# Performance work log

Hardware: AMD Instinct MI355X
Metric: run time of the kernel (lower is better)

Reference implementation:

```python
import jax, jax.numpy as jnp
import numpy as np

SOS = 1

def _gru_cell(x, h, Wih, Whh, bih, bhh):
    # PyTorch GRU cell: gates ordered (r, z, n)
    gi = x @ Wih.T + bih
    gh = h @ Whh.T + bhh
    ir, iz, inn = jnp.split(gi, 3, axis=-1)
    hr, hz, hn = jnp.split(gh, 3, axis=-1)
    r = jax.nn.sigmoid(ir + hr)
    z = jax.nn.sigmoid(iz + hz)
    n = jnp.tanh(inn + r * hn)
    return (1.0 - z) * n + z * h


def setup_inputs() -> dict:
    key = jax.random.key(0)
    ks = jax.random.split(key, 17)
    V, E, H, Lin, Tout, B, Lmax = 50000, 512, 512, 400, 100, 64, 400
    s = 0.05
    f = jax.random.normal
    return {
        "emb":     f(ks[0], (V, E)) * s,
        "enc_Wih": f(ks[1], (3 * H, E)) * s,
        "enc_Whh": f(ks[2], (3 * H, H)) * s,
        "enc_bih": f(ks[3], (3 * H,)) * s,
        "enc_bhh": f(ks[4], (3 * H,)) * s,
        "attn_W":  f(ks[5], (Lmax, 2 * H)) * s,
        "attn_b":  f(ks[6], (Lmax,)) * s,
        "comb_W":  f(ks[7], (H, 2 * H)) * s,
        "comb_b":  f(ks[8], (H,)) * s,
        "dec_Wih": f(ks[9], (3 * H, H)) * s,
        "dec_Whh": f(ks[10], (3 * H, H)) * s,
        "dec_bih": f(ks[11], (3 * H,)) * s,
        "dec_bhh": f(ks[12], (3 * H,)) * s,
        "out_W":   f(ks[13], (V, H)) * s,
        "out_b":   f(ks[14], (V,)) * s,
        "input_tensor":  jax.random.randint(ks[15], (Lin, B), 0, V),
        "target_tensor": jax.random.randint(ks[16], (Tout, B), 0, V),
    }


def reference(emb, enc_Wih, enc_Whh, enc_bih, enc_bhh, attn_W, attn_b,
              comb_W, comb_b, dec_Wih, dec_Whh, dec_bih, dec_bhh,
              out_W, out_b, input_tensor, target_tensor):
    B = input_tensor.shape[1]
    H = enc_Whh.shape[1]

    # ---- encoder: 1-layer GRU over [L, B, E] ----
    enc_x = emb[input_tensor]                      # [L, B, E]
    h0 = jnp.zeros((B, H), enc_x.dtype)
    def enc_step(h, x):
        h2 = _gru_cell(x, h, enc_Wih, enc_Whh, enc_bih, enc_bhh)
        return h2, h2
    h_enc, enc_out = jax.lax.scan(enc_step, h0, enc_x)   # enc_out: [L, B, H]
    enc0 = enc_out[0]                              # [B, H]; source's attn_applied[0] picks timestep 0

    # ---- decoder: teacher-forced, NLLLoss(mean) summed over steps ----
    dec_tokens = jnp.concatenate(
        [jnp.full((1, B), SOS, target_tensor.dtype), target_tensor[:-1]], axis=0)
    dec_x = emb[dec_tokens]                        # [T, B, H] (embed_size == hidden_size)

    def dec_step(h, xt):
        x, tgt = xt                                # x: [B, H], tgt: [B]
        a = jax.nn.softmax(jnp.concatenate([x, h], 1) @ attn_W.T + attn_b, axis=1)  # [B, Lmax]
        # faithful to source: elementwise broadcast picks enc_out[0] scaled by a[:, 0]
        ctx = enc0 * a[:, :1]                      # [B, H]
        c = jax.nn.relu(jnp.concatenate([x, ctx], 1) @ comb_W.T + comb_b)           # [B, H]
        h2 = _gru_cell(c, h, dec_Wih, dec_Whh, dec_bih, dec_bhh)
        logp = jax.nn.log_softmax(h2 @ out_W.T + out_b, axis=1)                     # [B, V]
        loss_t = -jnp.mean(jnp.take_along_axis(logp, tgt[:, None], axis=1))
        return h2, loss_t

    _, losses = jax.lax.scan(dec_step, h_enc, (dec_x, target_tensor))
    return jnp.sum(losses)
```

## Files before the change

### kernel.cpp

```cpp
#include <hip/hip_runtime.h>
#include <math.h>


typedef __attribute__((ext_vector_type(8))) short bh8;
typedef __attribute__((ext_vector_type(4))) float fv4;

__device__ __forceinline__ float b2f(short u) {
    union { unsigned int i; float f; } c;
    c.i = ((unsigned int)(unsigned short)u) << 16;
    return c.f;
}
__device__ __forceinline__ short f2b(float f) {
    union { float f; unsigned int u; } c;
    c.f = f;
    unsigned int r = (c.u + 0x7fffu + ((c.u >> 16) & 1u)) >> 16;
    return (short)r;
}
__device__ __forceinline__ bh8 ld8(const float* __restrict__ p) {
    bh8 r;
    #pragma unroll
    for (int j = 0; j < 8; ++j) r[j] = f2b(p[j]);
    return r;
}
__device__ __forceinline__ float sigmf(float x) { return 1.f / (1.f + expf(-x)); }

__device__ __forceinline__ fv4 mfma16(bh8 a, bh8 b, fv4 c) {
    return __builtin_amdgcn_mfma_f32_16x16x32_bf16(a, b, c, 0, 0, 0);
}

__device__ __forceinline__ void gridbar(unsigned int* bar, unsigned int target) {
    __syncthreads();
    if (threadIdx.x == 0) {
        __hip_atomic_fetch_add(bar, 1u, __ATOMIC_RELEASE, __HIP_MEMORY_SCOPE_AGENT);
        while (__hip_atomic_fetch_add(bar, 0u, __ATOMIC_RELAXED,
                                      __HIP_MEMORY_SCOPE_AGENT) < target) {
            __builtin_amdgcn_s_sleep(16);
        }
        __builtin_amdgcn_fence(__ATOMIC_ACQUIRE, "agent");
    }
    __syncthreads();
}

__global__ __launch_bounds__(256) void k_cvt(
    const float* __restrict__ s, short* __restrict__ d, int n)
{
    const int i = (blockIdx.x * 256 + threadIdx.x) * 4;
    if (i + 3 < n) {
        fv4 v = *(const fv4*)(s + i);
        short4 o;
        o.x = f2b(v[0]); o.y = f2b(v[1]); o.z = f2b(v[2]); o.w = f2b(v[3]);
        *(short4*)(d + i) = o;
    }
}

__global__ __launch_bounds__(256) void k_enc_persist(
    const float* __restrict__ emb, const int* __restrict__ input_t,
    const short* __restrict__ Wb,
    const float* __restrict__ Wih_f, const float* __restrict__ Whh_f,
    const float* __restrict__ bih, const float* __restrict__ bhh,
    float* __restrict__ h_f32, short* __restrict__ h_bf,
    float* __restrict__ enc0, unsigned int* __restrict__ bar)
{
    const int tid  = threadIdx.x;
    const int lane = tid & 63;
    const int wv   = tid >> 6;
    const int n0   = blockIdx.x * 16;
    const int b0   = wv * 16;
    const int l15  = lane & 15;
    const int ko   = lane >> 4;
    const int koff = ko * 8;
    const int brow = b0 + l15;
    const int n    = n0 + l15;

    for (int i = blockIdx.x * 256 + tid; i < 64 * 512; i += 32 * 256) {
        h_f32[i] = 0.f; h_bf[i] = 0;
    }
    gridbar(bar, 32u);

    const bh8 *Wrb = nullptr, *Wzb = nullptr, *Wnb = nullptr;
    const bh8 *Urb = nullptr, *Uzb = nullptr, *Unb = nullptr;
    const float *Wrf = nullptr, *Wzf = nullptr, *Wnf = nullptr;
    const float *Urf = nullptr, *Uzf = nullptr, *Unf = nullptr;
    if (Wb) {
        Wrb = (const bh8*)(Wb + (long long)(n + 0)    * 512) + ko;
        Wzb = (const bh8*)(Wb + (long long)(n + 512)  * 512) + ko;
        Wnb = (const bh8*)(Wb + (long long)(n + 1024) * 512) + ko;
        Urb = (const bh8*)(Wb + (long long)(n + 1536) * 512) + ko;
        Uzb = (const bh8*)(Wb + (long long)(n + 2048) * 512) + ko;
        Unb = (const bh8*)(Wb + (long long)(n + 2560) * 512) + ko;
    } else {
        Wrf = Wih_f + (long long)(n + 0)    * 512 + koff;
        Wzf = Wih_f + (long long)(n + 512)  * 512 + koff;
        Wnf = Wih_f + (long long)(n + 1024) * 512 + koff;
        Urf = Whh_f + (long long)(n + 0)    * 512 + koff;
        Uzf = Whh_f + (long long)(n + 512)  * 512 + koff;
        Unf = Whh_f + (long long)(n + 1024) * 512 + koff;
    }
    const float bir = bih[n], biz = bih[n + 512], bin = bih[n + 1024];
    const float bhr = bhh[n], bhz = bhh[n + 512], bhn = bhh[n + 1024];

    for (int t = 0; t < 400; ++t) {
        const float* hi  = h_f32 + (t & 1) * 32768;
        const short* hib = h_bf  + (t & 1) * 32768;
        float* ho  = h_f32 + ((t + 1) & 1) * 32768;
        short* hob = h_bf  + ((t + 1) & 1) * 32768;

        const int tok = input_t[t * 64 + brow];
        const float* Ap = emb + (long long)tok * 512 + koff;
        const bh8*  Hp  = (const bh8*)(hib + (long long)brow * 512) + ko;

        fv4 air = {0.f, 0.f, 0.f, 0.f};
        fv4 aiz = air, ain = air, ahr = air, ahz = air, ahn = air;
        if (Wb) {
            #pragma unroll 4
            for (int kk = 0; kk < 16; ++kk) {
                const bh8 a = ld8(Ap + kk * 32);
                const bh8 h = Hp[kk * 4];
                air = mfma16(a, Wrb[kk * 4], air);
                aiz = mfma16(a, Wzb[kk * 4], aiz);
                ain = mfma16(a, Wnb[kk * 4], ain);
                ahr = mfma16(h, Urb[kk * 4], ahr);
                ahz = mfma16(h, Uzb[kk * 4], ahz);
                ahn = mfma16(h, Unb[kk * 4], ahn);
            }
        } else {
            #pragma unroll 4
            for (int kk = 0; kk < 16; ++kk) {
                const bh8 a = ld8(Ap + kk * 32);
                const bh8 h = Hp[kk * 4];
                air = mfma16(a, ld8(Wrf + kk * 32), air);
                aiz = mfma16(a, ld8(Wzf + kk * 32), aiz);
                ain = mfma16(a, ld8(Wnf + kk * 32), ain);
                ahr = mfma16(h, ld8(Urf + kk * 32), ahr);
                ahz = mfma16(h, ld8(Uzf + kk * 32), ahz);
                ahn = mfma16(h, ld8(Unf + kk * 32), ahn);
            }
        }
        #pragma unroll
        for (int r = 0; r < 4; ++r) {
            const int b = b0 + ko * 4 + r;
            const float rr = sigmf(air[r] + bir + ahr[r] + bhr);
            const float zz = sigmf(aiz[r] + biz + ahz[r] + bhz);
            const float nn = tanhf(ain[r] + bin + rr * (ahn[r] + bhn));
            const float hold = hi[b * 512 + n];
            const float hnew = (1.f - zz) * nn + zz * hold;
            ho[b * 512 + n] = hnew;
            hob[b * 512 + n] = f2b(hnew);
            if (t == 0) enc0[b * 512 + n] = hnew;
        }
        gridbar(bar, 32u * (t + 2));
    }
}

struct SmAB { float sx[1024]; float red[256]; float red2[256]; };
struct SmD  { float sl[64][65]; };
union SMem { SmAB ab; SmD d; };

__device__ __forceinline__ void dec_lossred(
    const float* __restrict__ pm, const float* __restrict__ ps,
    const float* __restrict__ tlog, float* __restrict__ lacc,
    float* red, float* red2, int r, int tid)
{
    float m = -1e30f, s = 0.f;
    for (int i = tid; i < 782; i += 256) {
        const float m2 = pm[i * 64 + r];
        const float s2 = ps[i * 64 + r];
        if (m2 > m) { s = s * expf(m - m2) + s2; m = m2; }
        else        { s += s2 * expf(m2 - m); }
    }
    red[tid] = m; red2[tid] = s;
    __syncthreads();
    for (int st = 128; st > 0; st >>= 1) {
        if (tid < st) {
            const float m2 = red[tid + st], s2 = red2[tid + st];
            const float M = fmaxf(red[tid], m2);
            red2[tid] = red2[tid] * expf(red[tid] - M) + s2 * expf(m2 - M);
            red[tid] = M;
        }
        __syncthreads();
    }
    if (tid == 0) {
        const float logp = tlog[r] - (red[0] + logf(red2[0]));
        atomicAdd(lacc, -logp * (1.f / 64.f));
    }
    __syncthreads();
}

__global__ __launch_bounds__(256) void k_dec_persist(
    const float* __restrict__ emb, const float* __restrict__ enc0,
    const float* __restrict__ attn_W, const float* __restrict__ attn_b,
    const float* __restrict__ comb_W, const float* __restrict__ comb_b,
    const short* __restrict__ decWb,
    const float* __restrict__ dec_Wih, const float* __restrict__ dec_Whh,
    const float* __restrict__ dec_bih, const float* __restrict__ dec_bhh,
    const short* __restrict__ outWb, const float* __restrict__ outW,
    const float* __restrict__ outb, const int* __restrict__ target,
    float* __restrict__ h_f32, short* __restrict__ h_bf,
    short* __restrict__ c_bf, float* __restrict__ scores,
    float* __restrict__ pm, float* __restrict__ ps,
    float* __restrict__ tlog, float* __restrict__ lacc,
    unsigned int* __restrict__ bar2)
{
    __shared__ SMem sm;
    const int tid = threadIdx.x;
    const int bid = blockIdx.x;
    const int r   = bid >> 2;
    const int q   = bid & 3;
    unsigned int tgt = 0u;

    for (int t = 0; t < 100; ++t) {
        const float* hi  = h_f32 + (t & 1) * 32768;
        const short* hib = h_bf  + (t & 1) * 32768;
        float* ho  = h_f32 + ((t + 1) & 1) * 32768;
        short* hob = h_bf  + ((t + 1) & 1) * 32768;

        const int tok = (t == 0) ? 1 : target[(t - 1) * 64 + r];
        for (int k = tid; k < 512; k += 256) {
            sm.ab.sx[k]       = emb[(long long)tok * 512 + k];
            sm.ab.sx[512 + k] = hi[r * 512 + k];
        }
        if (q == 0 && t > 0)
            dec_lossred(pm, ps, tlog, lacc, sm.ab.red, sm.ab.red2, r, tid);
        __syncthreads();
        if (tid < 100) {
            const int nn = q * 100 + tid;
            const fv4* wrow = (const fv4*)(attn_W + (long long)nn * 1024);
            float s0 = 0.f, s1 = 0.f, s2 = 0.f, s3 = 0.f;
            for (int kc = 0; kc < 256; ++kc) {
                fv4 v = wrow[kc];
                s0 += v[0] * sm.ab.sx[kc * 4 + 0];
                s1 += v[1] * sm.ab.sx[kc * 4 + 1];
                s2 += v[2] * sm.ab.sx[kc * 4 + 2];
                s3 += v[3] * sm.ab.sx[kc * 4 + 3];
            }
            scores[r * 400 + nn] = (s0 + s1) + (s2 + s3) + attn_b[nn];
        }
        tgt += 256u; gridbar(bar2, tgt);

        {
            float m = -1e30f;
            for (int i = tid; i < 400; i += 256) m = fmaxf(m, scores[r * 400 + i]);
            sm.ab.red[tid] = m;
            __syncthreads();
            for (int st = 128; st > 0; st >>= 1) {
                if (tid < st) sm.ab.red[tid] = fmaxf(sm.ab.red[tid], sm.ab.red[tid + st]);
                __syncthreads();
            }
            m = sm.ab.red[0];
            __syncthreads();
            float ssum = 0.f;
            for (int i = tid; i < 400; i += 256) ssum += expf(scores[r * 400 + i] - m);
            sm.ab.red2[tid] = ssum;
            __syncthreads();
            for (int st = 128; st > 0; st >>= 1) {
                if (tid < st) sm.ab.red2[tid] += sm.ab.red2[tid + st];
                __syncthreads();
            }
            const float a0 = expf(scores[r * 400 + 0] - m) / sm.ab.red2[0];
            __syncthreads();
            for (int k = tid; k < 512; k += 256)
                sm.ab.sx[512 + k] = enc0[r * 512 + k] * a0;
            __syncthreads();
        }
        if (tid < 128) {
            const int j = q * 128 + tid;
            const fv4* wrow = (const fv4*)(comb_W + (long long)j * 1024);
            float s0 = 0.f, s1 = 0.f, s2 = 0.f, s3 = 0.f;
            for (int kc = 0; kc < 256; ++kc) {
                fv4 v = wrow[kc];
                s0 += v[0] * sm.ab.sx[kc * 4 + 0];
                s1 += v[1] * sm.ab.sx[kc * 4 + 1];
                s2 += v[2] * sm.ab.sx[kc * 4 + 2];
                s3 += v[3] * sm.ab.sx[kc * 4 + 3];
            }
            const float acc = (s0 + s1) + (s2 + s3) + comb_b[j];
            c_bf[r * 512 + j] = f2b(fmaxf(acc, 0.f));
        }
        tgt += 256u; gridbar(bar2, tgt);

        if (bid < 32) {
            const int lane = tid & 63;
            const int w    = bid * 4 + (tid >> 6);
            const int b0g  = (w & 3) * 16;
            const int n0g  = (w >> 2) * 16;
            const int l15  = lane & 15;
            const int ko   = lane >> 4;
            const int koff = ko * 8;
            const int brow = b0g + l15;
            const int n    = n0g + l15;

            const bh8* Ap = (const bh8*)(c_bf + (long long)brow * 512) + ko;
            const bh8* Hp = (const bh8*)(hib + (long long)brow * 512) + ko;

            fv4 air = {0.f, 0.f, 0.f, 0.f};
            fv4 aiz = air, ain = air, ahr = air, ahz = air, ahn = air;
            if (decWb) {
                const bh8* Wr = (const bh8*)(decWb + (long long)(n + 0)    * 512) + ko;
                const bh8* Wz = (const bh8*)(decWb + (long long)(n + 512)  * 512) + ko;
                const bh8* Wn = (const bh8*)(decWb + (long long)(n + 1024) * 512) + ko;
                const bh8* Ur = (const bh8*)(decWb + (long long)(n + 1536) * 512) + ko;
                const bh8* Uz = (const bh8*)(decWb + (long long)(n + 2048) * 512) + ko;
                const bh8* Un = (const bh8*)(decWb + (long long)(n + 2560) * 512) + ko;
                #pragma unroll 4
                for (int kk = 0; kk < 16; ++kk) {
                    const bh8 a = Ap[kk * 4];
                    const bh8 h = Hp[kk * 4];
                    air = mfma16(a, Wr[kk * 4], air);
                    aiz = mfma16(a, Wz[kk * 4], aiz);
                    ain = mfma16(a, Wn[kk * 4], ain);
                    ahr = mfma16(h, Ur[kk * 4], ahr);
                    ahz = mfma16(h, Uz[kk * 4], ahz);
                    ahn = mfma16(h, Un[kk * 4], ahn);
                }
            } else {
                const float* Wr = dec_Wih + (long long)(n + 0)    * 512 + koff;
                const float* Wz = dec_Wih + (long long)(n + 512)  * 512 + koff;
                const float* Wn = dec_Wih + (long long)(n + 1024) * 512 + koff;
                const float* Ur = dec_Whh + (long long)(n + 0)    * 512 + koff;
                const float* Uz = dec_Whh + (long long)(n + 512)  * 512 + koff;
                const float* Un = dec_Whh + (long long)(n + 1024) * 512 + koff;
                #pragma unroll 4
                for (int kk = 0; kk < 16; ++kk) {
                    const bh8 a = Ap[kk * 4];
                    const bh8 h = Hp[kk * 4];
                    air = mfma16(a, ld8(Wr + kk * 32), air);
                    aiz = mfma16(a, ld8(Wz + kk * 32), aiz);
                    ain = mfma16(a, ld8(Wn + kk * 32), ain);
                    ahr = mfma16(h, ld8(Ur + kk * 32), ahr);
                    ahz = mfma16(h, ld8(Uz + kk * 32), ahz);
                    ahn = mfma16(h, ld8(Un + kk * 32), ahn);
                }
            }
            const float bir = dec_bih[n], biz = dec_bih[n + 512], bin = dec_bih[n + 1024];
            const float bhr = dec_bhh[n], bhz = dec_bhh[n + 512], bhn = dec_bhh[n + 1024];
            #pragma unroll
            for (int rr = 0; rr < 4; ++rr) {
                const int b = b0g + ko * 4 + rr;
                const float rg = sigmf(air[rr] + bir + ahr[rr] + bhr);
                const float zg = sigmf(aiz[rr] + biz + ahz[rr] + bhz);
                const float ng = tanhf(ain[rr] + bin + rg * (ahn[rr] + bhn));
                const float hold = hi[b * 512 + n];
                const float hnew = (1.f - zg) * ng + zg * hold;
                ho[b * 512 + n] = hnew;
                hob[b * 512 + n] = f2b(hnew);
            }
        }
        tgt += 256u; gridbar(bar2, tgt);

        for (int ch = bid; ch < 782; ch += 256) {
            const int lane = tid & 63;
            const int wl   = tid >> 6;
            const int base = ch * 64;
            const int n0c  = base + wl * 16;
            const int l15  = lane & 15;
            const int ko   = lane >> 4;
            const int v    = n0c + l15;
            const int vcl  = (v < 50000) ? v : 49999;
            const bh8* A0 = (const bh8*)(hob + (long long)(0  + l15) * 512) + ko;
            const bh8* A1 = (const bh8*)(hob + (long long)(16 + l15) * 512) + ko;
            const bh8* A2 = (const bh8*)(hob + (long long)(32 + l15) * 512) + ko;
            const bh8* A3 = (const bh8*)(hob + (long long)(48 + l15) * 512) + ko;

            bh8 bb[16];
            if (outWb) {
                const bh8* Bp = (const bh8*)(outWb + (long long)vcl * 512) + ko;
                #pragma unroll
                for (int kk = 0; kk < 16; ++kk) bb[kk] = Bp[kk * 4];
            } else {
                const float* Bp = outW + (long long)vcl * 512 + ko * 8;
                #pragma unroll
                for (int kk = 0; kk < 16; ++kk) bb[kk] = ld8(Bp + kk * 32);
            }
            fv4 c0 = {0.f, 0.f, 0.f, 0.f};
            fv4 c1 = c0, c2 = c0, c3 = c0;
            #pragma unroll
            for (int kk = 0; kk < 16; ++kk) {
                c0 = mfma16(A0[kk * 4], bb[kk], c0);
                c1 = mfma16(A1[kk * 4], bb[kk], c1);
                c2 = mfma16(A2[kk * 4], bb[kk], c2);
                c3 = mfma16(A3[kk * 4], bb[kk], c3);
            }
            const float bv = outb[vcl];
            const int cc = wl * 16 + l15;
            const bool ok = (v < 50000);
            #pragma unroll
            for (int rr = 0; rr < 4; ++rr) {
                const int row = ko * 4 + rr;
                sm.d.sl[0  + row][cc] = ok ? (c0[rr] + bv) : -1e30f;
                sm.d.sl[16 + row][cc] = ok ? (c1[rr] + bv) : -1e30f;
                sm.d.sl[32 + row][cc] = ok ? (c2[rr] + bv) : -1e30f;
                sm.d.sl[48 + row][cc] = ok ? (c3[rr] + bv) : -1e30f;
            }
            __syncthreads();
            if (tid < 64) {
                const int b = tid;
                float m = -1e30f, s = 0.f;
                for (int cj = 0; cj < 64; ++cj) {
                    const float x = sm.d.sl[b][cj];
                    if (x > m) { s = s * expf(m - x) + 1.f; m = x; }
                    else       { s += expf(x - m); }
                }
                pm[ch * 64 + b] = m;
                ps[ch * 64 + b] = s;
                const int tg = target[t * 64 + b];
                const int rel = tg - base;
                if (rel >= 0 && rel < 64) tlog[b] = sm.d.sl[b][rel];
            }
            __syncthreads();
        }
        tgt += 256u; gridbar(bar2, tgt);
    }

    if (q == 0)
        dec_lossred(pm, ps, tlog, lacc, sm.ab.red, sm.ab.red2, r, tid);
}

__global__ __launch_bounds__(256) void k_gru1(
    const short* __restrict__ c_bf, const short* __restrict__ Wb,
    const float* __restrict__ Wih_f, const float* __restrict__ Whh_f,
    const float* __restrict__ bih, const float* __restrict__ bhh,
    const float* __restrict__ hi, const short* __restrict__ hib,
    float* __restrict__ ho, short* __restrict__ hob)
{
    const int tid  = threadIdx.x;
    const int lane = tid & 63;
    const int w    = blockIdx.x * 4 + (tid >> 6);
    const int b0   = (w & 3) * 16;
    const int n0   = (w >> 2) * 16;
    const int l15  = lane & 15;
    const int ko   = lane >> 4;
    const int koff = ko * 8;
    const int brow = b0 + l15;
    const int n    = n0 + l15;

    const bh8* Ap = (const bh8*)(c_bf + (long long)brow * 512) + ko;
    const bh8* Hp = (const bh8*)(hib + (long long)brow * 512) + ko;

    fv4 air = {0.f, 0.f, 0.f, 0.f};
    fv4 aiz = air, ain = air, ahr = air, ahz = air, ahn = air;
    if (Wb) {
        const bh8* Wr = (const bh8*)(Wb + (long long)(n + 0)    * 512) + ko;
        const bh8* Wz = (const bh8*)(Wb + (long long)(n + 512)  * 512) + ko;
        const bh8* Wn = (const bh8*)(Wb + (long long)(n + 1024) * 512) + ko;
        const bh8* Ur = (const bh8*)(Wb + (long long)(n + 1536) * 512) + ko;
        const bh8* Uz = (const bh8*)(Wb + (long long)(n + 2048) * 512) + ko;
        const bh8* Un = (const bh8*)(Wb + (long long)(n + 2560) * 512) + ko;
        #pragma unroll 4
        for (int kk = 0; kk < 16; ++kk) {
            const bh8 a = Ap[kk * 4];
            const bh8 h = Hp[kk * 4];
            air = mfma16(a, Wr[kk * 4], air);
            aiz = mfma16(a, Wz[kk * 4], aiz);
            ain = mfma16(a, Wn[kk * 4], ain);
            ahr = mfma16(h, Ur[kk * 4], ahr);
            ahz = mfma16(h, Uz[kk * 4], ahz);
            ahn = mfma16(h, Un[kk * 4], ahn);
        }
    } else {
        const float* Wr = Wih_f + (long long)(n + 0)    * 512 + koff;
        const float* Wz = Wih_f + (long long)(n + 512)  * 512 + koff;
        const float* Wn = Wih_f + (long long)(n + 1024) * 512 + koff;
        const float* Ur = Whh_f + (long long)(n + 0)    * 512 + koff;
        const float* Uz = Whh_f + (long long)(n + 512)  * 512 + koff;
        const float* Un = Whh_f + (long long)(n + 1024) * 512 + koff;
        #pragma unroll 4
        for (int kk = 0; kk < 16; ++kk) {
            const bh8 a = Ap[kk * 4];
            const bh8 h = Hp[kk * 4];
            air = mfma16(a, ld8(Wr + kk * 32), air);
            aiz = mfma16(a, ld8(Wz + kk * 32), aiz);
            ain = mfma16(a, ld8(Wn + kk * 32), ain);
            ahr = mfma16(h, ld8(Ur + kk * 32), ahr);
            ahz = mfma16(h, ld8(Uz + kk * 32), ahz);
            ahn = mfma16(h, ld8(Un + kk * 32), ahn);
        }
    }
    const float bir = bih[n], biz = bih[n + 512], bin = bih[n + 1024];
    const float bhr = bhh[n], bhz = bhh[n + 512], bhn = bhh[n + 1024];
    #pragma unroll
    for (int r = 0; r < 4; ++r) {
        const int b = b0 + ko * 4 + r;
        const float rr = sigmf(air[r] + bir + ahr[r] + bhr);
        const float zz = sigmf(aiz[r] + biz + ahz[r] + bhz);
        const float nn = tanhf(ain[r] + bin + rr * (ahn[r] + bhn));
        const float hold = hi[b * 512 + n];
        const float hnew = (1.f - zz) * nn + zz * hold;
        ho[b * 512 + n] = hnew;
        hob[b * 512 + n] = f2b(hnew);
    }
}

__global__ __launch_bounds__(256) void k_attncomb(
    const float* __restrict__ emb, const float* __restrict__ h_f32,
    const float* __restrict__ enc0,
    const float* __restrict__ attn_W, const float* __restrict__ attn_b,
    const float* __restrict__ comb_W, const float* __restrict__ comb_b,
    const int* __restrict__ target, int td, short* __restrict__ c_bf)
{
    __shared__ float sx[1024];
    __shared__ float sc[400];
    __shared__ float red[256];
    __shared__ float a0s;
    const int b = blockIdx.x;
    const int tid = threadIdx.x;
    const int tok = (td == 0) ? 1 : target[(td - 1) * 64 + b];
    for (int k = tid; k < 512; k += 256) {
        sx[k] = emb[(long long)tok * 512 + k];
        sx[512 + k] = h_f32[b * 512 + k];
    }
    __syncthreads();
    for (int nn = tid; nn < 400; nn += 256) {
        const fv4* wrow = (const fv4*)(attn_W + (long long)nn * 1024);
        float acc = 0.f;
        for (int kc = 0; kc < 256; ++kc) {
            fv4 v = wrow[kc];
            acc += v[0] * sx[kc * 4 + 0] + v[1] * sx[kc * 4 + 1]
                 + v[2] * sx[kc * 4 + 2] + v[3] * sx[kc * 4 + 3];
        }
        sc[nn] = acc + attn_b[nn];
    }
    __syncthreads();
    float m = -1e30f;
    for (int nn = tid; nn < 400; nn += 256) m = fmaxf(m, sc[nn]);
    red[tid] = m;
    __syncthreads();
    for (int s = 128; s > 0; s >>= 1) {
        if (tid < s) red[tid] = fmaxf(red[tid], red[tid + s]);
        __syncthreads();
    }
    m = red[0];
    __syncthreads();
    float ss = 0.f;
    for (int nn = tid; nn < 400; nn += 256) ss += expf(sc[nn] - m);
    red[tid] = ss;
    __syncthreads();
    for (int s = 128; s > 0; s >>= 1) {
        if (tid < s) red[tid] += red[tid + s];
        __syncthreads();
    }
    if (tid == 0) a0s = expf(sc[0] - m) / red[0];
    __syncthreads();
    const float a0b = a0s;
    for (int k = tid; k < 512; k += 256) sx[512 + k] = enc0[b * 512 + k] * a0b;
    __syncthreads();
    for (int j = tid; j < 512; j += 256) {
        const fv4* wrow = (const fv4*)(comb_W + (long long)j * 1024);
        float acc = 0.f;
        for (int kc = 0; kc < 256; ++kc) {
            fv4 v = wrow[kc];
            acc += v[0] * sx[kc * 4 + 0] + v[1] * sx[kc * 4 + 1]
                 + v[2] * sx[kc * 4 + 2] + v[3] * sx[kc * 4 + 3];
        }
        acc += comb_b[j];
        c_bf[b * 512 + j] = f2b(fmaxf(acc, 0.f));
    }
}

__global__ __launch_bounds__(256) void k_outloss(
    const short* __restrict__ h2bf,
    const short* __restrict__ outWb, const float* __restrict__ outW,
    const float* __restrict__ outb, const int* __restrict__ target,
    float* __restrict__ pm, float* __restrict__ ps, float* __restrict__ tlogit)
{
    __shared__ float sl[64][65];
    const int tid  = threadIdx.x;
    const int lane = tid & 63;
    const int wl   = tid >> 6;
    const int base = blockIdx.x * 64;
    const int n0   = base + wl * 16;
    const int l15  = lane & 15;
    const int ko   = lane >> 4;

    const int v    = n0 + l15;
    const int vcl  = (v < 50000) ? v : 49999;
    const bh8* A0 = (const bh8*)(h2bf + (long long)(0  + l15) * 512) + ko;
    const bh8* A1 = (const bh8*)(h2bf + (long long)(16 + l15) * 512) + ko;
    const bh8* A2 = (const bh8*)(h2bf + (long long)(32 + l15) * 512) + ko;
    const bh8* A3 = (const bh8*)(h2bf + (long long)(48 + l15) * 512) + ko;
    fv4 c0 = {0.f, 0.f, 0.f, 0.f};
    fv4 c1 = c0, c2 = c0, c3 = c0;
    if (outWb) {
        const bh8* Bp = (const bh8*)(outWb + (long long)vcl * 512) + ko;
        #pragma unroll 4
        for (int kk = 0; kk < 16; ++kk) {
            const bh8 bb = Bp[kk * 4];
            c0 = mfma16(A0[kk * 4], bb, c0);
            c1 = mfma16(A1[kk * 4], bb, c1);
            c2 = mfma16(A2[kk * 4], bb, c2);
            c3 = mfma16(A3[kk * 4], bb, c3);
        }
    } else {
        const float* Bp = outW + (long long)vcl * 512 + ko * 8;
        #pragma unroll 4
        for (int kk = 0; kk < 16; ++kk) {
            const bh8 bb = ld8(Bp + kk * 32);
            c0 = mfma16(A0[kk * 4], bb, c0);
            c1 = mfma16(A1[kk * 4], bb, c1);
            c2 = mfma16(A2[kk * 4], bb, c2);
            c3 = mfma16(A3[kk * 4], bb, c3);
        }
    }
    const float bv = outb[vcl];
    const int cc = wl * 16 + l15;
    const bool ok = (v < 50000);
    #pragma unroll
    for (int r = 0; r < 4; ++r) {
        const int row = ko * 4 + r;
        sl[0  + row][cc] = ok ? (c0[r] + bv) : -1e30f;
        sl[16 + row][cc] = ok ? (c1[r] + bv) : -1e30f;
        sl[32 + row][cc] = ok ? (c2[r] + bv) : -1e30f;
        sl[48 + row][cc] = ok ? (c3[r] + bv) : -1e30f;
    }
    __syncthreads();
    if (tid < 64) {
        const int b = tid;
        float m = -1e30f, s = 0.f;
        for (int c = 0; c < 64; ++c) {
            const float x = sl[b][c];
            if (x > m) { s = s * expf(m - x) + 1.f; m = x; }
            else       { s += expf(x - m); }
        }
        pm[blockIdx.x * 64 + b] = m;
        ps[blockIdx.x * 64 + b] = s;
        const int tg = target[b];
        const int rel = tg - base;
        if (rel >= 0 && rel < 64) tlogit[b] = sl[b][rel];
    }
}

__global__ __launch_bounds__(256) void k_lossred(
    const float* __restrict__ pm, const float* __restrict__ ps,
    const float* __restrict__ tlogit, float* __restrict__ loss_acc)
{
    __shared__ float rm[256], rs[256];
    const int b = blockIdx.x;
    const int tid = threadIdx.x;
    float m = -1e30f, s = 0.f;
    for (int i = tid; i < 782; i += 256) {
        const float m2 = pm[i * 64 + b];
        const float s2 = ps[i * 64 + b];
        if (m2 > m) { s = s * expf(m - m2) + s2; m = m2; }
        else        { s += s2 * expf(m2 - m); }
    }
    rm[tid] = m; rs[tid] = s;
    __syncthreads();
    for (int st = 128; st > 0; st >>= 1) {
        if (tid < st) {
            const float m2 = rm[tid + st], s2 = rs[tid + st];
            const float M = fmaxf(rm[tid], m2);
            rs[tid] = rs[tid] * expf(rm[tid] - M) + s2 * expf(m2 - M);
            rm[tid] = M;
        }
        __syncthreads();
    }
    if (tid == 0) {
        const float logp = tlogit[b] - (rm[0] + logf(rs[0]));
        atomicAdd(loss_acc, -logp * (1.f / 64.f));
    }
}

__global__ void k_init(float* h_f32_0, short* h_bf_0, float* loss_acc,
                       unsigned int* bar, unsigned int* bar2)
{
    const int i = blockIdx.x * 256 + threadIdx.x;
    if (i < 64 * 512) { h_f32_0[i] = 0.f; h_bf_0[i] = 0; }
    if (i == 0) { *loss_acc = 0.f; *bar = 0u; *bar2 = 0u; }
}

__global__ void k_final(const float* loss_acc, float* out)
{
    out[0] = *loss_acc;
}

extern "C" void kernel_launch(void* const* d_in, const int* in_sizes, int n_in,
                              void* d_out, int out_size, void* d_ws, size_t ws_size,
                              hipStream_t stream)
{
    const float* emb     = (const float*)d_in[0];
    const float* enc_Wih = (const float*)d_in[1];
    const float* enc_Whh = (const float*)d_in[2];
    const float* enc_bih = (const float*)d_in[3];
    const float* enc_bhh = (const float*)d_in[4];
    const float* attn_W  = (const float*)d_in[5];
    const float* attn_b  = (const float*)d_in[6];
    const float* comb_W  = (const float*)d_in[7];
    const float* comb_b  = (const float*)d_in[8];
    const float* dec_Wih = (const float*)d_in[9];
    const float* dec_Whh = (const float*)d_in[10];
    const float* dec_bih = (const float*)d_in[11];
    const float* dec_bhh = (const float*)d_in[12];
    const float* out_W   = (const float*)d_in[13];
    const float* out_b   = (const float*)d_in[14];
    const int*   input_t = (const int*)d_in[15];
    const int*   target_t= (const int*)d_in[16];

    char* ws = (char*)d_ws;
    float* h_f32  = (float*)(ws + 0);
    float* enc0   = (float*)(ws + 262144);
    short* h_bf   = (short*)(ws + 393216);
    short* c_bf   = (short*)(ws + 524288);
    float* lacc   = (float*)(ws + 589824);
    unsigned int* bar  = (unsigned int*)(ws + 590080);
    unsigned int* bar2 = (unsigned int*)(ws + 590208);
    float* pm     = (float*)(ws + 590336);
    float* ps     = (float*)(ws + 790528);
    float* tlog   = (float*)(ws + 990720);
    short* encWb  = (short*)(ws + 990976);
    float* scores = (float*)(ws + 990976);
    short* decWb  = (short*)(ws + 4136704);
    short* outWb  = (short*)(ws + 7282432);

    const bool tier1 = ws_size >= 7282432;
    const bool tier2 = ws_size >= 58482432;
    const bool fuse  = ws_size >= 1093376;

    k_init<<<128, 256, 0, stream>>>(h_f32, h_bf, lacc, bar, bar2);

    if (tier1) {
        k_cvt<<<768, 256, 0, stream>>>(enc_Wih, encWb, 786432);
        k_cvt<<<768, 256, 0, stream>>>(enc_Whh, encWb + 786432, 786432);
        k_cvt<<<768, 256, 0, stream>>>(dec_Wih, decWb, 786432);
        k_cvt<<<768, 256, 0, stream>>>(dec_Whh, decWb + 786432, 786432);
    }
    if (tier2) {
        k_cvt<<<25000, 256, 0, stream>>>(out_W, outWb, 25600000);
    }

    k_enc_persist<<<32, 256, 0, stream>>>(
        emb, input_t, tier1 ? encWb : nullptr, enc_Wih, enc_Whh,
        enc_bih, enc_bhh, h_f32, h_bf, enc0, bar);

    if (fuse) {
        k_dec_persist<<<256, 256, 0, stream>>>(
            emb, enc0, attn_W, attn_b, comb_W, comb_b,
            tier1 ? decWb : nullptr, dec_Wih, dec_Whh, dec_bih, dec_bhh,
            tier2 ? outWb : nullptr, out_W, out_b, target_t,
            h_f32, h_bf, c_bf, scores, pm, ps, tlog, lacc, bar2);
    } else {
        for (int td = 0; td < 100; ++td) {
            const float* hi  = h_f32 + (td & 1) * 32768;
            const short* hib = h_bf  + (td & 1) * 32768;
            float* ho  = h_f32 + ((td + 1) & 1) * 32768;
            short* hob = h_bf  + ((td + 1) & 1) * 32768;
            k_attncomb<<<64, 256, 0, stream>>>(emb, hi, enc0, attn_W, attn_b,
                                               comb_W, comb_b, target_t, td, c_bf);
            k_gru1<<<32, 256, 0, stream>>>(c_bf, tier1 ? decWb : nullptr,
                                           dec_Wih, dec_Whh, dec_bih, dec_bhh,
                                           hi, hib, ho, hob);
            k_outloss<<<782, 256, 0, stream>>>(hob, tier2 ? outWb : nullptr, out_W,
                                               out_b, target_t + td * 64,
                                               pm, ps, tlog);
            k_lossred<<<64, 256, 0, stream>>>(pm, ps, tlog, lacc);
        }
    }

    k_final<<<1, 1, 0, stream>>>(lacc, (float*)d_out);
}
```

Measured before the change: 28.27 ms.

## Move output projection out of recurrent loop into one batched kernel over all steps

The persistent decoder now runs only the recurrent part (attention, combine, GRU) on 64 blocks with two grid barriers per step, and stores every step's hidden state in bf16. A separate kernel then computes the vocabulary projection and partial log-softmax for all 100 steps in parallel (800 blocks). A final kernel reduces the partial results into the loss. This removes the huge per-step vocabulary GEMM and its barriers from the serial critical path. It also converts only part of out_W to bf16 under a smaller workspace budget and falls back to fp32 loads for the remaining chunks.

```diff
diff --git a/kernel.cpp b/kernel.cpp
--- a/kernel.cpp
+++ b/kernel.cpp
@@ -4,6 +4,9 @@
 
 typedef __attribute__((ext_vector_type(8))) short bh8;
 typedef __attribute__((ext_vector_type(4))) float fv4;
+
+#define NSL 8
+#define CONVCH 640
 
 __device__ __forceinline__ float b2f(short u) {
     union { unsigned int i; float f; } c;
@@ -152,131 +155,88 @@
     }
 }
 
-struct SmAB { float sx[1024]; float red[256]; float red2[256]; };
-struct SmD  { float sl[64][65]; };
-union SMem { SmAB ab; SmD d; };
-
-__device__ __forceinline__ void dec_lossred(
-    const float* __restrict__ pm, const float* __restrict__ ps,
-    const float* __restrict__ tlog, float* __restrict__ lacc,
-    float* red, float* red2, int r, int tid)
-{
-    float m = -1e30f, s = 0.f;
-    for (int i = tid; i < 782; i += 256) {
-        const float m2 = pm[i * 64 + r];
-        const float s2 = ps[i * 64 + r];
-        if (m2 > m) { s = s * expf(m - m2) + s2; m = m2; }
-        else        { s += s2 * expf(m2 - m); }
-    }
-    red[tid] = m; red2[tid] = s;
-    __syncthreads();
-    for (int st = 128; st > 0; st >>= 1) {
-        if (tid < st) {
-            const float m2 = red[tid + st], s2 = red2[tid + st];
-            const float M = fmaxf(red[tid], m2);
-            red2[tid] = red2[tid] * expf(red[tid] - M) + s2 * expf(m2 - M);
-            red[tid] = M;
-        }
-        __syncthreads();
-    }
-    if (tid == 0) {
-        const float logp = tlog[r] - (red[0] + logf(red2[0]));
-        atomicAdd(lacc, -logp * (1.f / 64.f));
-    }
-    __syncthreads();
-}
-
-__global__ __launch_bounds__(256) void k_dec_persist(
+__global__ __launch_bounds__(256) void k_dec2(
     const float* __restrict__ emb, const float* __restrict__ enc0,
     const float* __restrict__ attn_W, const float* __restrict__ attn_b,
     const float* __restrict__ comb_W, const float* __restrict__ comb_b,
     const short* __restrict__ decWb,
     const float* __restrict__ dec_Wih, const float* __restrict__ dec_Whh,
     const float* __restrict__ dec_bih, const float* __restrict__ dec_bhh,
-    const short* __restrict__ outWb, const float* __restrict__ outW,
-    const float* __restrict__ outb, const int* __restrict__ target,
-    float* __restrict__ h_f32, short* __restrict__ h_bf,
-    short* __restrict__ c_bf, float* __restrict__ scores,
-    float* __restrict__ pm, float* __restrict__ ps,
-    float* __restrict__ tlog, float* __restrict__ lacc,
+    const int* __restrict__ target,
+    float* __restrict__ h,
+    const float* __restrict__ h0,
+    const short* __restrict__ h0b,
+    short* __restrict__ c_bf, short* __restrict__ Hall,
     unsigned int* __restrict__ bar2)
 {
-    __shared__ SMem sm;
+    __shared__ __align__(16) float sx[1024];
+    __shared__ float sc[400];
+    __shared__ float red[256];
+    __shared__ float a0s;
     const int tid = threadIdx.x;
     const int bid = blockIdx.x;
-    const int r   = bid >> 2;
-    const int q   = bid & 3;
     unsigned int tgt = 0u;
 
     for (int t = 0; t < 100; ++t) {
-        const float* hi  = h_f32 + (t & 1) * 32768;
-        const short* hib = h_bf  + (t & 1) * 32768;
-        float* ho  = h_f32 + ((t + 1) & 1) * 32768;
-        short* hob = h_bf  + ((t + 1) & 1) * 32768;
-
-        const int tok = (t == 0) ? 1 : target[(t - 1) * 64 + r];
-        for (int k = tid; k < 512; k += 256) {
-            sm.ab.sx[k]       = emb[(long long)tok * 512 + k];
-            sm.ab.sx[512 + k] = hi[r * 512 + k];
-        }
-        if (q == 0 && t > 0)
-            dec_lossred(pm, ps, tlog, lacc, sm.ab.red, sm.ab.red2, r, tid);
-        __syncthreads();
-        if (tid < 100) {
-            const int nn = q * 100 + tid;
-            const fv4* wrow = (const fv4*)(attn_W + (long long)nn * 1024);
-            float s0 = 0.f, s1 = 0.f, s2 = 0.f, s3 = 0.f;
-            for (int kc = 0; kc < 256; ++kc) {
-                fv4 v = wrow[kc];
-                s0 += v[0] * sm.ab.sx[kc * 4 + 0];
-                s1 += v[1] * sm.ab.sx[kc * 4 + 1];
-                s2 += v[2] * sm.ab.sx[kc * 4 + 2];
-                s3 += v[3] * sm.ab.sx[kc * 4 + 3];
-            }
-            scores[r * 400 + nn] = (s0 + s1) + (s2 + s3) + attn_b[nn];
-        }
-        tgt += 256u; gridbar(bar2, tgt);
-
         {
+            const int r = bid;
+            const float* hsrc = (t == 0) ? h0 : h;
+            const int tok = (t == 0) ? 1 : target[(t - 1) * 64 + r];
+            for (int k = tid; k < 512; k += 256) {
+                sx[k]       = emb[(long long)tok * 512 + k];
+                sx[512 + k] = hsrc[r * 512 + k];
+            }
+            __syncthreads();
+            for (int nn = tid; nn < 400; nn += 256) {
+                const fv4* wrow = (const fv4*)(attn_W + (long long)nn * 1024);
+                float s0 = 0.f, s1 = 0.f, s2 = 0.f, s3 = 0.f;
+                for (int kc = 0; kc < 256; ++kc) {
+                    const fv4 v = wrow[kc];
+                    const fv4 xv = *(const fv4*)(sx + kc * 4);
+                    s0 += v[0] * xv[0]; s1 += v[1] * xv[1];
+                    s2 += v[2] * xv[2]; s3 += v[3] * xv[3];
+                }
+                sc[nn] = (s0 + s1) + (s2 + s3) + attn_b[nn];
+            }
+            __syncthreads();
             float m = -1e30f;
-            for (int i = tid; i < 400; i += 256) m = fmaxf(m, scores[r * 400 + i]);
-            sm.ab.red[tid] = m;
+            for (int nn = tid; nn < 400; nn += 256) m = fmaxf(m, sc[nn]);
+            red[tid] = m;
             __syncthreads();
-            for (int st = 128; st > 0; st >>= 1) {
-                if (tid < st) sm.ab.red[tid] = fmaxf(sm.ab.red[tid], sm.ab.red[tid + st]);
+            for (int s = 128; s > 0; s >>= 1) {
+                if (tid < s) red[tid] = fmaxf(red[tid], red[tid + s]);
                 __syncthreads();
             }
-            m = sm.ab.red[0];
+            m = red[0];
             __syncthreads();
-            float ssum = 0.f;
-            for (int i = tid; i < 400; i += 256) ssum += expf(scores[r * 400 + i] - m);
-            sm.ab.red2[tid] = ssum;
+            float ss = 0.f;
+            for (int nn = tid; nn < 400; nn += 256) ss += expf(sc[nn] - m);
+            red[tid] = ss;
             __syncthreads();
-            for (int st = 128; st > 0; st >>= 1) {
-                if (tid < st) sm.ab.red2[tid] += sm.ab.red2[tid + st];
+            for (int s = 128; s > 0; s >>= 1) {
+                if (tid < s) red[tid] += red[tid + s];
                 __syncthreads();
             }
-            const float a0 = expf(scores[r * 400 + 0] - m) / sm.ab.red2[0];
+            if (tid == 0) a0s = expf(sc[0] - m) / red[0];
             __syncthreads();
+            const float a0 = a0s;
             for (int k = tid; k < 512; k += 256)
-                sm.ab.sx[512 + k] = enc0[r * 512 + k] * a0;
+                sx[512 + k] = enc0[r * 512 + k] * a0;
             __syncthreads();
-        }
-        if (tid < 128) {
-            const int j = q * 128 + tid;
-            const fv4* wrow = (const fv4*)(comb_W + (long long)j * 1024);
-            float s0 = 0.f, s1 = 0.f, s2 = 0.f, s3 = 0.f;
-            for (int kc = 0; kc < 256; ++kc) {
-                fv4 v = wrow[kc];
-                s0 += v[0] * sm.ab.sx[kc * 4 + 0];
-                s1 += v[1] * sm.ab.sx[kc * 4 + 1];
-                s2 += v[2] * sm.ab.sx[kc * 4 + 2];
-                s3 += v[3] * sm.ab.sx[kc * 4 + 3];
-            }
-            const float acc = (s0 + s1) + (s2 + s3) + comb_b[j];
-            c_bf[r * 512 + j] = f2b(fmaxf(acc, 0.f));
-        }
-        tgt += 256u; gridbar(bar2, tgt);
+            for (int j = tid; j < 512; j += 256) {
+                const fv4* wrow = (const fv4*)(comb_W + (long long)j * 1024);
+                float s0 = 0.f, s1 = 0.f, s2 = 0.f, s3 = 0.f;
+                for (int kc = 0; kc < 256; ++kc) {
+                    const fv4 v = wrow[kc];
+                    const fv4 xv = *(const fv4*)(sx + kc * 4);
+                    s0 += v[0] * xv[0]; s1 += v[1] * xv[1];
+                    s2 += v[2] * xv[2]; s3 += v[3] * xv[3];
+                }
+                const float acc = (s0 + s1) + (s2 + s3) + comb_b[j];
+                c_bf[r * 512 + j] = f2b(fmaxf(acc, 0.f));
+            }
+        }
+        tgt += 64u; gridbar(bar2, tgt);
 
         if (bid < 32) {
             const int lane = tid & 63;
@@ -289,8 +249,10 @@
             const int brow = b0g + l15;
             const int n    = n0g + l15;
 
+            const short* Hprev = (t == 0) ? h0b : (Hall + (long long)(t - 1) * 32768);
+            const float* hsrc  = (t == 0) ? h0  : h;
             const bh8* Ap = (const bh8*)(c_bf + (long long)brow * 512) + ko;
-            const bh8* Hp = (const bh8*)(hib + (long long)brow * 512) + ko;
+            const bh8* Hp = (const bh8*)(Hprev + (long long)brow * 512) + ko;
 
             fv4 air = {0.f, 0.f, 0.f, 0.f};
             fv4 aiz = air, ain = air, ahr = air, ahz = air, ahn = air;
@@ -304,13 +266,13 @@
                 #pragma unroll 4
                 for (int kk = 0; kk < 16; ++kk) {
                     const bh8 a = Ap[kk * 4];
-                    const bh8 h = Hp[kk * 4];
-                    air = mfma16(a, Wr[kk * 4], air);
-                    aiz = mfma16(a, Wz[kk * 4], aiz);
-                    ain = mfma16(a, Wn[kk * 4], ain);
-                    ahr = mfma16(h, Ur[kk * 4], ahr);
-                    ahz = mfma16(h, Uz[kk * 4], ahz);
-                    ahn = mfma16(h, Un[kk * 4], ahn);
+                    const bh8 hh = Hp[kk * 4];
+                    air = mfma16(a,  Wr[kk * 4], air);
+                    aiz = mfma16(a,  Wz[kk * 4], aiz);
+                    ain = mfma16(a,  Wn[kk * 4], ain);
+                    ahr = mfma16(hh, Ur[kk * 4], ahr);
+                    ahz = mfma16(hh, Uz[kk * 4], ahz);
+                    ahn = mfma16(hh, Un[kk * 4], ahn);
                 }
             } else {
                 const float* Wr = dec_Wih + (long long)(n + 0)    * 512 + koff;
@@ -322,97 +284,149 @@
                 #pragma unroll 4
                 for (int kk = 0; kk < 16; ++kk) {
                     const bh8 a = Ap[kk * 4];
-                    const bh8 h = Hp[kk * 4];
-                    air = mfma16(a, ld8(Wr + kk * 32), air);
-                    aiz = mfma16(a, ld8(Wz + kk * 32), aiz);
-                    ain = mfma16(a, ld8(Wn + kk * 32), ain);
-                    ahr = mfma16(h, ld8(Ur + kk * 32), ahr);
-                    ahz = mfma16(h, ld8(Uz + kk * 32), ahz);
-                    ahn = mfma16(h, ld8(Un + kk * 32), ahn);
+                    const bh8 hh = Hp[kk * 4];
+                    air = mfma16(a,  ld8(Wr + kk * 32), air);
+                    aiz = mfma16(a,  ld8(Wz + kk * 32), aiz);
+                    ain = mfma16(a,  ld8(Wn + kk * 32), ain);
+                    ahr = mfma16(hh, ld8(Ur + kk * 32), ahr);
+                    ahz = mfma16(hh, ld8(Uz + kk * 32), ahz);
+                    ahn = mfma16(hh, ld8(Un + kk * 32), ahn);
                 }
             }
             const float bir = dec_bih[n], biz = dec_bih[n + 512], bin = dec_bih[n + 1024];
             const float bhr = dec_bhh[n], bhz = dec_bhh[n + 512], bhn = dec_bhh[n + 1024];
+            short* Ht = Hall + (long long)t * 32768;
             #pragma unroll
             for (int rr = 0; rr < 4; ++rr) {
                 const int b = b0g + ko * 4 + rr;
                 const float rg = sigmf(air[rr] + bir + ahr[rr] + bhr);
                 const float zg = sigmf(aiz[rr] + biz + ahz[rr] + bhz);
                 const float ng = tanhf(ain[rr] + bin + rg * (ahn[rr] + bhn));
-                const float hold = hi[b * 512 + n];
+                const float hold = hsrc[b * 512 + n];
                 const float hnew = (1.f - zg) * ng + zg * hold;
-                ho[b * 512 + n] = hnew;
-                hob[b * 512 + n] = f2b(hnew);
-            }
-        }
-        tgt += 256u; gridbar(bar2, tgt);
-
-        for (int ch = bid; ch < 782; ch += 256) {
-            const int lane = tid & 63;
-            const int wl   = tid >> 6;
-            const int base = ch * 64;
-            const int n0c  = base + wl * 16;
-            const int l15  = lane & 15;
-            const int ko   = lane >> 4;
-            const int v    = n0c + l15;
-            const int vcl  = (v < 50000) ? v : 49999;
-            const bh8* A0 = (const bh8*)(hob + (long long)(0  + l15) * 512) + ko;
-            const bh8* A1 = (const bh8*)(hob + (long long)(16 + l15) * 512) + ko;
-            const bh8* A2 = (const bh8*)(hob + (long long)(32 + l15) * 512) + ko;
-            const bh8* A3 = (const bh8*)(hob + (long long)(48 + l15) * 512) + ko;
-
-            bh8 bb[16];
-            if (outWb) {
-                const bh8* Bp = (const bh8*)(outWb + (long long)vcl * 512) + ko;
-                #pragma unroll
-                for (int kk = 0; kk < 16; ++kk) bb[kk] = Bp[kk * 4];
-            } else {
-                const float* Bp = outW + (long long)vcl * 512 + ko * 8;
-                #pragma unroll
-                for (int kk = 0; kk < 16; ++kk) bb[kk] = ld8(Bp + kk * 32);
-            }
-            fv4 c0 = {0.f, 0.f, 0.f, 0.f};
-            fv4 c1 = c0, c2 = c0, c3 = c0;
+                h[b * 512 + n] = hnew;
+                Ht[b * 512 + n] = f2b(hnew);
+            }
+        }
+        tgt += 64u; gridbar(bar2, tgt);
+    }
+}
+
+__global__ __launch_bounds__(256) void k_outbatch(
+    const short* __restrict__ Hall,
+    const short* __restrict__ outWb, const float* __restrict__ outW,
+    const float* __restrict__ outb, const int* __restrict__ target,
+    float* __restrict__ pm2, float* __restrict__ ps2, float* __restrict__ tlog2)
+{
+    __shared__ float sl[64][65];
+    __shared__ float mm[4][64], sm[4][64], tm[4][64];
+    const int tid  = threadIdx.x;
+    const int s    = blockIdx.x & 7;
+    const int t    = blockIdx.x >> 3;
+    const int lane = tid & 63;
+    const int wl   = tid >> 6;
+    const int l15  = lane & 15;
+    const int ko   = lane >> 4;
+    const short* Ht = Hall + (long long)t * 32768;
+    const bh8* A0 = (const bh8*)(Ht + (long long)(0  + l15) * 512) + ko;
+    const bh8* A1 = (const bh8*)(Ht + (long long)(16 + l15) * 512) + ko;
+    const bh8* A2 = (const bh8*)(Ht + (long long)(32 + l15) * 512) + ko;
+    const bh8* A3 = (const bh8*)(Ht + (long long)(48 + l15) * 512) + ko;
+
+    const int row = tid & 63;
+    const int seg = tid >> 6;
+    const int tg  = target[t * 64 + row];
+    float lm = -1e30f, ls = 0.f, tcap = -1e30f;
+
+    const int ch0 = s * 98;
+    const int ch1 = (ch0 + 98 < 782) ? (ch0 + 98) : 782;
+    for (int ch = ch0; ch < ch1; ++ch) {
+        const int base = ch * 64;
+        const int n0c  = base + wl * 16;
+        const int v    = n0c + l15;
+        const int vcl  = (v < 50000) ? v : 49999;
+        bh8 bb[16];
+        if (outWb && ch < CONVCH) {
+            const bh8* Bp = (const bh8*)(outWb + (long long)vcl * 512) + ko;
             #pragma unroll
-            for (int kk = 0; kk < 16; ++kk) {
-                c0 = mfma16(A0[kk * 4], bb[kk], c0);
-                c1 = mfma16(A1[kk * 4], bb[kk], c1);
-                c2 = mfma16(A2[kk * 4], bb[kk], c2);
-                c3 = mfma16(A3[kk * 4], bb[kk], c3);
-            }
-            const float bv = outb[vcl];
-            const int cc = wl * 16 + l15;
-            const bool ok = (v < 50000);
+            for (int kk = 0; kk < 16; ++kk) bb[kk] = Bp[kk * 4];
+        } else {
+            const float* Bp = outW + (long long)vcl * 512 + ko * 8;
             #pragma unroll
-            for (int rr = 0; rr < 4; ++rr) {
-                const int row = ko * 4 + rr;
-                sm.d.sl[0  + row][cc] = ok ? (c0[rr] + bv) : -1e30f;
-                sm.d.sl[16 + row][cc] = ok ? (c1[rr] + bv) : -1e30f;
-                sm.d.sl[32 + row][cc] = ok ? (c2[rr] + bv) : -1e30f;
-                sm.d.sl[48 + row][cc] = ok ? (c3[rr] + bv) : -1e30f;
-            }
-            __syncthreads();
-            if (tid < 64) {
-                const int b = tid;
-                float m = -1e30f, s = 0.f;
-                for (int cj = 0; cj < 64; ++cj) {
-                    const float x = sm.d.sl[b][cj];
-                    if (x > m) { s = s * expf(m - x) + 1.f; m = x; }
-                    else       { s += expf(x - m); }
-                }
-                pm[ch * 64 + b] = m;
-                ps[ch * 64 + b] = s;
-                const int tg = target[t * 64 + b];
-                const int rel = tg - base;
-                if (rel >= 0 && rel < 64) tlog[b] = sm.d.sl[b][rel];
-            }
-            __syncthreads();
-        }
-        tgt += 256u; gridbar(bar2, tgt);
-    }
-
-    if (q == 0)
-        dec_lossred(pm, ps, tlog, lacc, sm.ab.red, sm.ab.red2, r, tid);
+            for (int kk = 0; kk < 16; ++kk) bb[kk] = ld8(Bp + kk * 32);
+        }
+        fv4 c0 = {0.f, 0.f, 0.f, 0.f};
+        fv4 c1 = c0, c2 = c0, c3 = c0;
+        #pragma unroll
+        for (int kk = 0; kk < 16; ++kk) {
+            c0 = mfma16(A0[kk * 4], bb[kk], c0);
+            c1 = mfma16(A1[kk * 4], bb[kk], c1);
+            c2 = mfma16(A2[kk * 4], bb[kk], c2);
+            c3 = mfma16(A3[kk * 4], bb[kk], c3);
+        }
+        const float bv = outb[vcl];
+        const int cc = wl * 16 + l15;
+        const bool ok = (v < 50000);
+        #pragma unroll
+        for (int rr = 0; rr < 4; ++rr) {
+            const int rw = ko * 4 + rr;
+            sl[0  + rw][cc] = ok ? (c0[rr] + bv) : -1e30f;
+            sl[16 + rw][cc] = ok ? (c1[rr] + bv) : -1e30f;
+            sl[32 + rw][cc] = ok ? (c2[rr] + bv) : -1e30f;
+            sl[48 + rw][cc] = ok ? (c3[rr] + bv) : -1e30f;
+        }
+        __syncthreads();
+        #pragma unroll
+        for (int j = 0; j < 16; ++j) {
+            const float x = sl[row][seg * 16 + j];
+            if (x > lm) { ls = ls * expf(lm - x) + 1.f; lm = x; }
+            else        { ls += expf(x - lm); }
+            if (base + seg * 16 + j == tg) tcap = x;
+        }
+        __syncthreads();
+    }
+    mm[seg][row] = lm; sm[seg][row] = ls; tm[seg][row] = tcap;
+    __syncthreads();
+    if (tid < 64) {
+        float M = mm[0][tid], S = sm[0][tid], T = tm[0][tid];
+        #pragma unroll
+        for (int g = 1; g < 4; ++g) {
+            const float m2 = mm[g][tid], s2 = sm[g][tid];
+            const float Mx = fmaxf(M, m2);
+            S = S * expf(M - Mx) + s2 * expf(m2 - Mx);
+            M = Mx;
+            T = fmaxf(T, tm[g][tid]);
+        }
+        pm2[((long long)t * NSL + s) * 64 + tid] = M;
+        ps2[((long long)t * NSL + s) * 64 + tid] = S;
+        if (T > -5e29f) tlog2[t * 64 + tid] = T;
+    }
+}
+
+__global__ __launch_bounds__(64) void k_lossfinal(
+    const float* __restrict__ pm2, const float* __restrict__ ps2,
+    const float* __restrict__ tlog2, float* __restrict__ lacc)
+{
+    __shared__ float rs[64];
+    const int t = blockIdx.x;
+    const int b = threadIdx.x;
+    float M = pm2[((long long)t * NSL) * 64 + b];
+    float S = ps2[((long long)t * NSL) * 64 + b];
+    for (int g = 1; g < NSL; ++g) {
+        const float m2 = pm2[((long long)t * NSL + g) * 64 + b];
+        const float s2 = ps2[((long long)t * NSL + g) * 64 + b];
+        const float Mx = fmaxf(M, m2);
+        S = S * expf(M - Mx) + s2 * expf(m2 - Mx);
+        M = Mx;
+    }
+    const float lp = tlog2[t * 64 + b] - (M + logf(S));
+    rs[b] = lp;
+    __syncthreads();
+    for (int st = 32; st > 0; st >>= 1) {
+        if (b < st) rs[b] += rs[b + st];
+        __syncthreads();
+    }
+    if (b == 0) atomicAdd(lacc, -rs[0] * (1.f / 64.f));
 }
 
 __global__ __launch_bounds__(256) void k_gru1(
@@ -659,12 +673,11 @@
     }
 }
 
-__global__ void k_init(float* h_f32_0, short* h_bf_0, float* loss_acc,
-                       unsigned int* bar, unsigned int* bar2)
-{
-    const int i = blockIdx.x * 256 + threadIdx.x;
-    if (i < 64 * 512) { h_f32_0[i] = 0.f; h_bf_0[i] = 0; }
-    if (i == 0) { *loss_acc = 0.f; *bar = 0u; *bar2 = 0u; }
+__global__ void k_init(float* loss_acc, unsigned int* bar, unsigned int* bar2)
+{
+    if (threadIdx.x == 0 && blockIdx.x == 0) {
+        *loss_acc = 0.f; *bar = 0u; *bar2 = 0u;
+    }
 }
 
 __global__ void k_final(const float* loss_acc, float* out)
@@ -695,64 +708,92 @@
     const int*   target_t= (const int*)d_in[16];
 
     char* ws = (char*)d_ws;
+
     float* h_f32  = (float*)(ws + 0);
-    float* enc0   = (float*)(ws + 262144);
-    short* h_bf   = (short*)(ws + 393216);
-    short* c_bf   = (short*)(ws + 524288);
-    float* lacc   = (float*)(ws + 589824);
-    unsigned int* bar  = (unsigned int*)(ws + 590080);
-    unsigned int* bar2 = (unsigned int*)(ws + 590208);
-    float* pm     = (float*)(ws + 590336);
-    float* ps     = (float*)(ws + 790528);
-    float* tlog   = (float*)(ws + 990720);
-    short* encWb  = (short*)(ws + 990976);
-    float* scores = (float*)(ws + 990976);
-    short* decWb  = (short*)(ws + 4136704);
-    short* outWb  = (short*)(ws + 7282432);
-
-    const bool tier1 = ws_size >= 7282432;
-    const bool tier2 = ws_size >= 58482432;
-    const bool fuse  = ws_size >= 1093376;
-
-    k_init<<<128, 256, 0, stream>>>(h_f32, h_bf, lacc, bar, bar2);
-
-    if (tier1) {
+    float* enc0   = (float*)(ws + 131072);
+    short* c_bf   = (short*)(ws + 262144);
+    short* hm1    = (short*)(ws + 327680);
+    float* lacc   = (float*)(ws + 393216);
+    unsigned int* bar  = (unsigned int*)(ws + 393472);
+    unsigned int* bar2 = (unsigned int*)(ws + 393728);
+    float* pm2    = (float*)(ws + 393984);
+    float* ps2    = (float*)(ws + 598784);
+    float* tlog2  = (float*)(ws + 803584);
+    short* Hall   = (short*)(ws + 829184);
+    float* he_f32 = (float*)(ws + 7382784);
+    short* he_bf  = (short*)(ws + 7644928);
+    short* encWb  = (short*)(ws + 7776000);
+    short* decWb  = (short*)(ws + 10921728);
+    short* outWb3 = (short*)(ws + 14067456);
+    (void)hm1;
+
+    const bool fuse  = ws_size >= 14067456;
+    const bool tierP = ws_size >= 14067456 + 41943040ull;
+
+    if (fuse) {
+        k_init<<<1, 64, 0, stream>>>(lacc, bar, bar2);
         k_cvt<<<768, 256, 0, stream>>>(enc_Wih, encWb, 786432);
         k_cvt<<<768, 256, 0, stream>>>(enc_Whh, encWb + 786432, 786432);
         k_cvt<<<768, 256, 0, stream>>>(dec_Wih, decWb, 786432);
         k_cvt<<<768, 256, 0, stream>>>(dec_Whh, decWb + 786432, 786432);
-    }
-    if (tier2) {
-        k_cvt<<<25000, 256, 0, stream>>>(out_W, outWb, 25600000);
-    }
-
+        if (tierP)
+            k_cvt<<<20480, 256, 0, stream>>>(out_W, outWb3, 20971520);
+
+        k_enc_persist<<<32, 256, 0, stream>>>(
+            emb, input_t, encWb, enc_Wih, enc_Whh,
+            enc_bih, enc_bhh, he_f32, he_bf, enc0, bar);
+
+        k_dec2<<<64, 256, 0, stream>>>(
+            emb, enc0, attn_W, attn_b, comb_W, comb_b,
+            decWb, dec_Wih, dec_Whh, dec_bih, dec_bhh, target_t,
+            h_f32, he_f32, he_bf, c_bf, Hall, bar2);
+
+        k_outbatch<<<100 * NSL, 256, 0, stream>>>(
+            Hall, tierP ? outWb3 : nullptr, out_W, out_b, target_t,
+            pm2, ps2, tlog2);
+        k_lossfinal<<<100, 64, 0, stream>>>(pm2, ps2, tlog2, lacc);
+        k_final<<<1, 1, 0, stream>>>(lacc, (float*)d_out);
+        return;
+    }
+
+    float* f_h_f32  = (float*)(ws + 0);
+    float* f_enc0   = (float*)(ws + 262144);
+    short* f_h_bf   = (short*)(ws + 393216);
+    short* f_c_bf   = (short*)(ws + 524288);
+    float* f_lacc   = (float*)(ws + 589824);
+    unsigned int* f_bar  = (unsigned int*)(ws + 590080);
+    unsigned int* f_bar2 = (unsigned int*)(ws + 590208);
+    float* f_pm     = (float*)(ws + 590336);
+    float* f_ps     = (float*)(ws + 790528);
+    float* f_tlog   = (float*)(ws + 990720);
+    short* f_encWb  = (short*)(ws + 990976);
+    short* f_decWb  = (short*)(ws + 4136704);
+    const bool f_tier1 = ws_size >= 7282432;
+
+    k_init<<<1, 64, 0, stream>>>(f_lacc, f_bar, f_bar2);
+    if (f_tier1) {
+        k_cvt<<<768, 256, 0, stream>>>(enc_Wih, f_encWb, 786432);
+        k_cvt<<<768, 256, 0, stream>>>(enc_Whh, f_encWb + 786432, 786432);
+        k_cvt<<<768, 256, 0, stream>>>(dec_Wih, f_decWb, 786432);
+        k_cvt<<<768, 256, 0, stream>>>(dec_Whh, f_decWb + 786432, 786432);
+    }
     k_enc_persist<<<32, 256, 0, stream>>>(
-        emb, input_t, tier1 ? encWb : nullptr, enc_Wih, enc_Whh,
-        enc_bih, enc_bhh, h_f32, h_bf, enc0, bar);
-
-    if (fuse) {
-        k_dec_persist<<<256, 256, 0, stream>>>(
-            emb, enc0, attn_W, attn_b, comb_W, comb_b,
-            tier1 ? decWb : nullptr, dec_Wih, dec_Whh, dec_bih, dec_bhh,
-            tier2 ? outWb : nullptr, out_W, out_b, target_t,
-            h_f32, h_bf, c_bf, scores, pm, ps, tlog, lacc, bar2);
-    } else {
-        for (int td = 0; td < 100; ++td) {
-            const float* hi  = h_f32 + (td & 1) * 32768;
-            const short* hib = h_bf  + (td & 1) * 32768;
-            float* ho  = h_f32 + ((td + 1) & 1) * 32768;
-            short* hob = h_bf  + ((td + 1) & 1) * 32768;
-            k_attncomb<<<64, 256, 0, stream>>>(emb, hi, enc0, attn_W, attn_b,
-                                               comb_W, comb_b, target_t, td, c_bf);
-            k_gru1<<<32, 256, 0, stream>>>(c_bf, tier1 ? decWb : nullptr,
-                                           dec_Wih, dec_Whh, dec_bih, dec_bhh,
-                                           hi, hib, ho, hob);
-            k_outloss<<<782, 256, 0, stream>>>(hob, tier2 ? outWb : nullptr, out_W,
-                                               out_b, target_t + td * 64,
-                                               pm, ps, tlog);
-            k_lossred<<<64, 256, 0, stream>>>(pm, ps, tlog, lacc);
-        }
-    }
-
-    k_final<<<1, 1, 0, stream>>>(lacc, (float*)d_out);
-}
+        emb, input_t, f_tier1 ? f_encWb : nullptr, enc_Wih, enc_Whh,
+        enc_bih, enc_bhh, f_h_f32, f_h_bf, f_enc0, f_bar);
+    for (int td = 0; td < 100; ++td) {
+        const float* hi  = f_h_f32 + (td & 1) * 32768;
+        const short* hib = f_h_bf  + (td & 1) * 32768;
+        float* ho  = f_h_f32 + ((td + 1) & 1) * 32768;
+        short* hob = f_h_bf  + ((td + 1) & 1) * 32768;
+        k_attncomb<<<64, 256, 0, stream>>>(emb, hi, f_enc0, attn_W, attn_b,
+                                           comb_W, comb_b, target_t, td, f_c_bf);
+        k_gru1<<<32, 256, 0, stream>>>(f_c_bf, f_tier1 ? f_decWb : nullptr,
+                                       dec_Wih, dec_Whh, dec_bih, dec_bhh,
+                                       hi, hib, ho, hob);
+        k_outloss<<<782, 256, 0, stream>>>(hob, nullptr, out_W,
+                                           out_b, target_t + td * 64,
+                                           f_pm, f_ps, f_tlog);
+        k_lossred<<<64, 256, 0, stream>>>(f_pm, f_ps, f_tlog, f_lacc);
+    }
+    k_final<<<1, 1, 0, stream>>>(f_lacc, (float*)d_out);
+}
```

Measured after the change: 29.77 ms. 5.3% more time.
